# Kernel tuning notes

Measured on AMD Instinct MI355X. Metric: run time of the kernel, lower is better.

Reference implementation:

```python
import jax, jax.numpy as jnp
import numpy as np

B, S, D, H = 2, 2048, 1024, 16
HD = D // H  # head size 64

def setup_inputs() -> dict:
    key = jax.random.key(0)
    ks = jax.random.split(key, 7)
    sc = 1.0 / np.sqrt(D)
    return {
        "batch_data": jax.random.normal(ks[0], (B, S, D), dtype=jnp.float32),
        "Wq": jax.random.normal(ks[1], (D, D), dtype=jnp.float32) * sc,
        "bq": jnp.zeros((D,), dtype=jnp.float32),
        "Wk": jax.random.normal(ks[2], (D, D), dtype=jnp.float32) * sc,
        "bk": jnp.zeros((D,), dtype=jnp.float32),
        "Wv": jax.random.normal(ks[3], (D, D), dtype=jnp.float32) * sc,
        "bv": jnp.zeros((D,), dtype=jnp.float32),
    }

def _split_heads(x):
    # [B,S,D] -> [B,H,S,HD]
    b, s, _ = x.shape
    return x.reshape(b, s, H, HD).transpose(0, 2, 1, 3)

def reference(batch_data, Wq, bq, Wk, bk, Wv, bv):
    q = _split_heads(batch_data @ Wq + bq)
    k = _split_heads(batch_data @ Wk + bk)
    v = _split_heads(batch_data @ Wv + bv)
    scores = jnp.einsum('bhqd,bhkd->bhqk', q, k) / jnp.sqrt(jnp.float32(HD))
    probs = jax.nn.softmax(scores, axis=-1)
    ctx = jnp.einsum('bhqk,bhkd->bhqd', probs, v)  # [B,H,S,HD]
    ctx = ctx.transpose(0, 2, 1, 3).reshape(batch_data.shape[0], batch_data.shape[1], D)
    return jnp.mean(ctx, axis=1)  # mean pool over sequence -> [B,D]
```

## Files before the change

kernel.cpp:

```cpp
#include <hip/hip_runtime.h>
#include <hip/hip_bf16.h>
#include <stdint.h>

#define B_  2
#define S_  2048
#define D_  1024
#define H_  16
#define HD_ 64

typedef __attribute__((ext_vector_type(8)))  __bf16 bf16x8;
typedef __attribute__((ext_vector_type(4)))  __bf16 bf16x4;
typedef __attribute__((ext_vector_type(2)))  __bf16 bf16x2;
typedef __attribute__((ext_vector_type(4)))  float  f32x4;
typedef __attribute__((ext_vector_type(16))) float  f32x16;
typedef __attribute__((ext_vector_type(4)))  uint32_t u32x4;

#define QSCALE 0.18033688011112042f

__device__ __forceinline__ void gload16(const void* g, void* l) {
  __builtin_amdgcn_global_load_lds(
      (__attribute__((address_space(1))) void*)(uintptr_t)g,
      (__attribute__((address_space(3))) void*)(uintptr_t)l,
      16, 0, 0);
}

__device__ __forceinline__ uint32_t pkbf(float a, float b) {
  bf16x2 p; p[0] = (__bf16)a; p[1] = (__bf16)b;
  return __builtin_bit_cast(uint32_t, p);
}

__global__ __launch_bounds__(256) void zero_out_k(float* out) {
  int i = blockIdx.x * 256 + threadIdx.x;
  if (i < B_ * D_) out[i] = 0.0f;
}

__global__ __launch_bounds__(256) void convert_x(const float* __restrict__ x,
                                                 __bf16* __restrict__ xb) {
  int i = blockIdx.x * 256 + threadIdx.x;
  float4 v = ((const float4*)x)[i];
  bf16x4 o;
  o[0] = (__bf16)v.x; o[1] = (__bf16)v.y; o[2] = (__bf16)v.z; o[3] = (__bf16)v.w;
  ((bf16x4*)xb)[i] = o;
}

__global__ __launch_bounds__(256) void transpose_w(const float* __restrict__ wq,
                                                   const float* __restrict__ wk,
                                                   const float* __restrict__ wv,
                                                   __bf16* __restrict__ wt) {
  __shared__ float tile[32][33];
  const float* w = (blockIdx.z == 0) ? wq : (blockIdx.z == 1 ? wk : wv);
  __bf16* o = wt + (size_t)blockIdx.z * D_ * D_;
  int k0 = blockIdx.y * 32, n0 = blockIdx.x * 32;
  int tx = threadIdx.x, ty = threadIdx.y;
  for (int i = 0; i < 4; ++i)
    tile[ty + 8 * i][tx] = w[(size_t)(k0 + ty + 8 * i) * D_ + n0 + tx];
  __syncthreads();
  for (int i = 0; i < 4; ++i)
    o[(size_t)(n0 + ty + 8 * i) * D_ + k0 + tx] = (__bf16)tile[tx][ty + 8 * i];
}

__global__ __launch_bounds__(256, 3) void gemm_qkv(
    const __bf16* __restrict__ xb, const __bf16* __restrict__ wt,
    const float* __restrict__ bq, const float* __restrict__ bk,
    const float* __restrict__ bv, __bf16* __restrict__ qh,
    __bf16* __restrict__ kh, __bf16* __restrict__ vt) {
  constexpr int K = 1024;
  __shared__ __attribute__((aligned(16))) __bf16 lA[128 * 64];
  __shared__ __attribute__((aligned(16))) __bf16 lB[128 * 64];

  const int z = blockIdx.z;
  const __bf16* w = wt + (size_t)z * K * D_;
  const float* bias = (z == 0) ? bq : (z == 1 ? bk : bv);
  const int t = threadIdx.x;
  const int lane = t & 63;
  const int wid = t >> 6;
  const int quad = lane >> 4;
  const int col = lane & 15;
  const int m0 = blockIdx.x * 128;
  const int n0 = blockIdx.y * 128;
  const int wr = (wid >> 1) * 64;
  const int wc = (wid & 1) * 64;

  const int gc = (t & 7) ^ ((t >> 3) & 7);

  f32x4 acc[4][4] = {};

  if (z < 2) {
    for (int kt = 0; kt < K / 64; ++kt) {
      __syncthreads();
      for (int r = 0; r < 4; ++r) {
        int row = r * 32 + (t >> 3);
        gload16(xb + (size_t)(m0 + row) * K + kt * 64 + gc * 8,
                (char*)lA + r * 4096 + t * 16);
        gload16(w + (size_t)(n0 + row) * K + kt * 64 + gc * 8,
                (char*)lB + r * 4096 + t * 16);
      }
      __syncthreads();
      for (int ks = 0; ks < 2; ++ks) {
        bf16x8 fw[4], fx[4];
        for (int i = 0; i < 4; ++i) {
          int n = wr + i * 16 + col;
          int ch = (ks * 4 + quad) ^ (n & 7);
          fw[i] = *(const bf16x8*)((const char*)lB + n * 128 + ch * 16);
        }
        for (int j = 0; j < 4; ++j) {
          int m = wc + j * 16 + col;
          int ch = (ks * 4 + quad) ^ (m & 7);
          fx[j] = *(const bf16x8*)((const char*)lA + m * 128 + ch * 16);
        }
        for (int i = 0; i < 4; ++i)
          for (int j = 0; j < 4; ++j)
            acc[i][j] = __builtin_amdgcn_mfma_f32_16x16x32_bf16(
                fw[i], fx[j], acc[i][j], 0, 0, 0);
      }
    }
    const float scale = (z == 0) ? QSCALE : 1.0f;
    __bf16* dst = (z == 0) ? qh : kh;
    for (int i = 0; i < 4; ++i) {
      int gnb = n0 + wr + i * 16 + quad * 4;
      float4 bi = *(const float4*)(bias + gnb);
      int h = gnb >> 6, hd = gnb & 63;
      for (int j = 0; j < 4; ++j) {
        int gm = m0 + wc + j * 16 + col;
        int b = gm >> 11, s = gm & 2047;
        bf16x4 pk;
        pk[0] = (__bf16)((acc[i][j][0] + bi.x) * scale);
        pk[1] = (__bf16)((acc[i][j][1] + bi.y) * scale);
        pk[2] = (__bf16)((acc[i][j][2] + bi.z) * scale);
        pk[3] = (__bf16)((acc[i][j][3] + bi.w) * scale);
        *(bf16x4*)(dst + ((size_t)(b * H_ + h) * S_ + s) * HD_ + hd) = pk;
      }
    }
  } else {
    for (int kt = 0; kt < K / 64; ++kt) {
      __syncthreads();
      for (int r = 0; r < 4; ++r) {
        int row = r * 32 + (t >> 3);
        gload16(xb + (size_t)(m0 + row) * K + kt * 64 + gc * 8,
                (char*)lA + r * 4096 + t * 16);
        gload16(w + (size_t)(n0 + row) * K + kt * 64 + gc * 8,
                (char*)lB + r * 4096 + t * 16);
      }
      __syncthreads();
      for (int ks = 0; ks < 2; ++ks) {
        bf16x8 fx[4], fw[4];
        for (int i = 0; i < 4; ++i) {
          int m = wr + i * 16 + col;
          int ch = (ks * 4 + quad) ^ (m & 7);
          fx[i] = *(const bf16x8*)((const char*)lA + m * 128 + ch * 16);
        }
        for (int j = 0; j < 4; ++j) {
          int n = wc + j * 16 + col;
          int ch = (ks * 4 + quad) ^ (n & 7);
          fw[j] = *(const bf16x8*)((const char*)lB + n * 128 + ch * 16);
        }
        for (int i = 0; i < 4; ++i)
          for (int j = 0; j < 4; ++j)
            acc[i][j] = __builtin_amdgcn_mfma_f32_16x16x32_bf16(
                fx[i], fw[j], acc[i][j], 0, 0, 0);
      }
    }
    for (int i = 0; i < 4; ++i) {
      int gmb = m0 + wr + i * 16 + quad * 4;
      int b = gmb >> 11, s = gmb & 2047;
      for (int j = 0; j < 4; ++j) {
        int gn = n0 + wc + j * 16 + col;
        int h = gn >> 6, hd = gn & 63;
        float bi = bias[gn];
        bf16x4 pk;
        pk[0] = (__bf16)(acc[i][j][0] + bi);
        pk[1] = (__bf16)(acc[i][j][1] + bi);
        pk[2] = (__bf16)(acc[i][j][2] + bi);
        pk[3] = (__bf16)(acc[i][j][3] + bi);
        *(bf16x4*)(vt + ((size_t)(b * H_ + h) * HD_ + hd) * S_ + s) = pk;
      }
    }
  }
}

__global__ __launch_bounds__(256, 2) void attn(const __bf16* __restrict__ qh,
                                               const __bf16* __restrict__ kh,
                                               const __bf16* __restrict__ vt,
                                               float* __restrict__ out) {
  __shared__ __attribute__((aligned(16))) __bf16 lK[128 * 64];
  __shared__ __attribute__((aligned(16))) __bf16 lV[64 * 128];

  const int t = threadIdx.x;
  const int lane = t & 63;
  const int wid = t >> 6;
  const int half = lane >> 5;
  const int q31 = lane & 31;
  const int bh = blockIdx.x;
  const int q0w = blockIdx.y * 128 + wid * 32;

  const __bf16* qbase = qh + (size_t)bh * S_ * HD_;
  const __bf16* kbase = kh + (size_t)bh * S_ * HD_;
  const __bf16* vbase = vt + (size_t)bh * HD_ * S_;

  bf16x8 aq[4];
  for (int ks = 0; ks < 4; ++ks)
    aq[ks] = *(const bf16x8*)(qbase + (size_t)(q0w + q31) * HD_ + ks * 16 + half * 8);

  f32x16 o[2] = {};
  float lsum = 0.f;

  const int kslot = t & 7,  kgc = kslot ^ ((t >> 3) & 7);
  const int vslot = t & 15, vgc = vslot ^ ((t >> 4) & 15);

  for (int kt = 0; kt < S_ / 128; ++kt) {
    __syncthreads();
    for (int r = 0; r < 4; ++r) {
      int row = r * 32 + (t >> 3);
      gload16(kbase + (size_t)(kt * 128 + row) * HD_ + kgc * 8,
              (char*)lK + r * 4096 + t * 16);
      int rowv = r * 16 + (t >> 4);
      gload16(vbase + (size_t)rowv * S_ + kt * 128 + vgc * 8,
              (char*)lV + r * 4096 + t * 16);
    }
    __syncthreads();

    for (int st = 0; st < 4; ++st) {
      f32x16 sc = {};
      for (int ks = 0; ks < 4; ++ks) {
        int row = st * 32 + q31;
        int ch = (ks * 2 + half) ^ (row & 7);
        bf16x8 fk = *(const bf16x8*)((const char*)lK + row * 128 + ch * 16);
        sc = __builtin_amdgcn_mfma_f32_32x32x16_bf16(fk, aq[ks], sc, 0, 0, 0);
      }

      float e[16];
      for (int r = 0; r < 16; ++r) e[r] = exp2f(sc[r]);
      for (int r = 0; r < 16; ++r) lsum += e[r];
      uint32_t pk[8], x[8];
      for (int p = 0; p < 8; ++p) pk[p] = pkbf(e[2 * p], e[2 * p + 1]);
      for (int p = 0; p < 8; ++p) x[p] = __shfl_xor((int)pk[p], 32);

      bool h1 = (half != 0);
      u32x4 f0 = {h1 ? x[2] : pk[0], h1 ? x[3] : pk[1],
                  h1 ? pk[2] : x[0], h1 ? pk[3] : x[1]};
      u32x4 f1 = {h1 ? x[6] : pk[4], h1 ? x[7] : pk[5],
                  h1 ? pk[6] : x[4], h1 ? pk[7] : x[5]};
      bf16x8 Fa = __builtin_bit_cast(bf16x8, f0);
      bf16x8 Fb = __builtin_bit_cast(bf16x8, f1);

      for (int hdt = 0; hdt < 2; ++hdt) {
        int rowv = hdt * 32 + q31;
        int ch0 = (st * 4 + half) ^ (rowv & 15);
        int ch1 = (st * 4 + 2 + half) ^ (rowv & 15);
        bf16x8 fv0 = *(const bf16x8*)((const char*)lV + rowv * 256 + ch0 * 16);
        bf16x8 fv1 = *(const bf16x8*)((const char*)lV + rowv * 256 + ch1 * 16);
        o[hdt] = __builtin_amdgcn_mfma_f32_32x32x16_bf16(fv0, Fa, o[hdt], 0, 0, 0);
        o[hdt] = __builtin_amdgcn_mfma_f32_32x32x16_bf16(fv1, Fb, o[hdt], 0, 0, 0);
      }
    }
  }

  float ltot = lsum + __shfl_xor(lsum, 32);
  float linv = 1.0f / ltot;
  const int b = bh >> 4, h = bh & 15;
  for (int hdt = 0; hdt < 2; ++hdt)
    for (int r = 0; r < 16; ++r) {
      float v = o[hdt][r] * linv;
      v += __shfl_xor(v, 1);
      v += __shfl_xor(v, 2);
      v += __shfl_xor(v, 4);
      v += __shfl_xor(v, 8);
      v += __shfl_xor(v, 16);
      if (q31 == 0) {
        int hd = hdt * 32 + (r & 3) + 8 * (r >> 2) + 4 * half;
        atomicAdd(out + (size_t)b * D_ + h * HD_ + hd, v * (1.0f / S_));
      }
    }
}

extern "C" void kernel_launch(void* const* d_in, const int* in_sizes, int n_in,
                              void* d_out, int out_size, void* d_ws, size_t ws_size,
                              hipStream_t stream) {
  const float* x  = (const float*)d_in[0];
  const float* Wq = (const float*)d_in[1];
  const float* bq = (const float*)d_in[2];
  const float* Wk = (const float*)d_in[3];
  const float* bk = (const float*)d_in[4];
  const float* Wv = (const float*)d_in[5];
  const float* bv = (const float*)d_in[6];
  float* out = (float*)d_out;

  char* ws = (char*)d_ws;
  __bf16* qh = (__bf16*)(ws);
  __bf16* kh = (__bf16*)(ws + ((size_t)8  << 20));
  __bf16* vt = (__bf16*)(ws + ((size_t)16 << 20));
  __bf16* xb = (__bf16*)(ws + ((size_t)24 << 20));
  __bf16* wt = (__bf16*)(ws + ((size_t)32 << 20));

  zero_out_k<<<dim3((B_ * D_ + 255) / 256), dim3(256), 0, stream>>>(out);
  convert_x<<<dim3((B_ * S_ * D_) / 1024), dim3(256), 0, stream>>>(x, xb);
  transpose_w<<<dim3(32, 32, 3), dim3(32, 8), 0, stream>>>(Wq, Wk, Wv, wt);
  gemm_qkv<<<dim3(32, 8, 3), dim3(256), 0, stream>>>(xb, wt, bq, bk, bv, qh, kh, vt);
  attn<<<dim3(B_ * H_, S_ / 128), dim3(256), 0, stream>>>(qh, kh, vt, out);
}
```

Baseline: 191.5 us.

## Double-buffer K/V tiles in LDS and split MFMA accumulator chains

```diff
diff --git a/kernel.cpp b/kernel.cpp
--- a/kernel.cpp
+++ b/kernel.cpp
@@ -182,16 +182,15 @@
                                                const __bf16* __restrict__ kh,
                                                const __bf16* __restrict__ vt,
                                                float* __restrict__ out) {
-  __shared__ __attribute__((aligned(16))) __bf16 lK[128 * 64];
-  __shared__ __attribute__((aligned(16))) __bf16 lV[64 * 128];
+  __shared__ __attribute__((aligned(16))) __bf16 lK[2][128 * 64];
+  __shared__ __attribute__((aligned(16))) __bf16 lV[2][64 * 128];
 
   const int t = threadIdx.x;
   const int lane = t & 63;
-  const int wid = t >> 6;
   const int half = lane >> 5;
   const int q31 = lane & 31;
   const int bh = blockIdx.x;
-  const int q0w = blockIdx.y * 128 + wid * 32;
+  const int q0w = blockIdx.y * 128 + (t >> 6) * 32;
 
   const __bf16* qbase = qh + (size_t)bh * S_ * HD_;
   const __bf16* kbase = kh + (size_t)bh * S_ * HD_;
@@ -201,40 +200,54 @@
   for (int ks = 0; ks < 4; ++ks)
     aq[ks] = *(const bf16x8*)(qbase + (size_t)(q0w + q31) * HD_ + ks * 16 + half * 8);
 
-  f32x16 o[2] = {};
-  float lsum = 0.f;
-
-  const int kslot = t & 7,  kgc = kslot ^ ((t >> 3) & 7);
-  const int vslot = t & 15, vgc = vslot ^ ((t >> 4) & 15);
-
-  for (int kt = 0; kt < S_ / 128; ++kt) {
-    __syncthreads();
+  const int kgc = (t & 7) ^ ((t >> 3) & 7);
+  const int vgc = (t & 15) ^ ((t >> 4) & 15);
+
+  auto stage = [&](int kt, int buf) {
     for (int r = 0; r < 4; ++r) {
       int row = r * 32 + (t >> 3);
       gload16(kbase + (size_t)(kt * 128 + row) * HD_ + kgc * 8,
-              (char*)lK + r * 4096 + t * 16);
+              (char*)&lK[buf][0] + r * 4096 + t * 16);
       int rowv = r * 16 + (t >> 4);
       gload16(vbase + (size_t)rowv * S_ + kt * 128 + vgc * 8,
-              (char*)lV + r * 4096 + t * 16);
-    }
+              (char*)&lV[buf][0] + r * 4096 + t * 16);
+    }
+  };
+
+  f32x16 o[2][2] = {};
+  float lsum = 0.f;
+
+  stage(0, 0);
+
+  for (int kt = 0; kt < S_ / 128; ++kt) {
+    const int cur = kt & 1;
     __syncthreads();
-
+    if (kt + 1 < S_ / 128) stage(kt + 1, cur ^ 1);
+
+    f32x16 sc[4] = {};
+#pragma unroll
     for (int st = 0; st < 4; ++st) {
-      f32x16 sc = {};
+      int row = st * 32 + q31;
+#pragma unroll
       for (int ks = 0; ks < 4; ++ks) {
-        int row = st * 32 + q31;
         int ch = (ks * 2 + half) ^ (row & 7);
-        bf16x8 fk = *(const bf16x8*)((const char*)lK + row * 128 + ch * 16);
-        sc = __builtin_amdgcn_mfma_f32_32x32x16_bf16(fk, aq[ks], sc, 0, 0, 0);
-      }
-
+        bf16x8 fk = *(const bf16x8*)((const char*)&lK[cur][0] + row * 128 + ch * 16);
+        sc[st] = __builtin_amdgcn_mfma_f32_32x32x16_bf16(fk, aq[ks], sc[st], 0, 0, 0);
+      }
+    }
+
+#pragma unroll
+    for (int st = 0; st < 4; ++st) {
       float e[16];
-      for (int r = 0; r < 16; ++r) e[r] = exp2f(sc[r]);
+#pragma unroll
+      for (int r = 0; r < 16; ++r) e[r] = exp2f(sc[st][r]);
+#pragma unroll
       for (int r = 0; r < 16; ++r) lsum += e[r];
       uint32_t pk[8], x[8];
+#pragma unroll
       for (int p = 0; p < 8; ++p) pk[p] = pkbf(e[2 * p], e[2 * p + 1]);
+#pragma unroll
       for (int p = 0; p < 8; ++p) x[p] = __shfl_xor((int)pk[p], 32);
-
       bool h1 = (half != 0);
       u32x4 f0 = {h1 ? x[2] : pk[0], h1 ? x[3] : pk[1],
                   h1 ? pk[2] : x[0], h1 ? pk[3] : x[1]};
@@ -242,15 +255,17 @@
                   h1 ? pk[6] : x[4], h1 ? pk[7] : x[5]};
       bf16x8 Fa = __builtin_bit_cast(bf16x8, f0);
       bf16x8 Fb = __builtin_bit_cast(bf16x8, f1);
-
+#pragma unroll
       for (int hdt = 0; hdt < 2; ++hdt) {
         int rowv = hdt * 32 + q31;
         int ch0 = (st * 4 + half) ^ (rowv & 15);
         int ch1 = (st * 4 + 2 + half) ^ (rowv & 15);
-        bf16x8 fv0 = *(const bf16x8*)((const char*)lV + rowv * 256 + ch0 * 16);
-        bf16x8 fv1 = *(const bf16x8*)((const char*)lV + rowv * 256 + ch1 * 16);
-        o[hdt] = __builtin_amdgcn_mfma_f32_32x32x16_bf16(fv0, Fa, o[hdt], 0, 0, 0);
-        o[hdt] = __builtin_amdgcn_mfma_f32_32x32x16_bf16(fv1, Fb, o[hdt], 0, 0, 0);
+        bf16x8 fv0 = *(const bf16x8*)((const char*)&lV[cur][0] + rowv * 256 + ch0 * 16);
+        bf16x8 fv1 = *(const bf16x8*)((const char*)&lV[cur][0] + rowv * 256 + ch1 * 16);
+        o[hdt][st & 1] = __builtin_amdgcn_mfma_f32_32x32x16_bf16(
+            fv0, Fa, o[hdt][st & 1], 0, 0, 0);
+        o[hdt][st & 1] = __builtin_amdgcn_mfma_f32_32x32x16_bf16(
+            fv1, Fb, o[hdt][st & 1], 0, 0, 0);
       }
     }
   }
@@ -258,9 +273,11 @@
   float ltot = lsum + __shfl_xor(lsum, 32);
   float linv = 1.0f / ltot;
   const int b = bh >> 4, h = bh & 15;
+#pragma unroll
   for (int hdt = 0; hdt < 2; ++hdt)
+#pragma unroll
     for (int r = 0; r < 16; ++r) {
-      float v = o[hdt][r] * linv;
+      float v = (o[hdt][0][r] + o[hdt][1][r]) * linv;
       v += __shfl_xor(v, 1);
       v += __shfl_xor(v, 2);
       v += __shfl_xor(v, 4);
```

Result: no change. 189.7 us (-1.0%).

## Double-buffer QKV GEMM loads and split attention across two key chunks

Applied to the files above, without the earlier changes.

```diff
diff --git a/kernel.cpp b/kernel.cpp
--- a/kernel.cpp
+++ b/kernel.cpp
@@ -65,8 +65,9 @@
     const float* __restrict__ bv, __bf16* __restrict__ qh,
     __bf16* __restrict__ kh, __bf16* __restrict__ vt) {
   constexpr int K = 1024;
-  __shared__ __attribute__((aligned(16))) __bf16 lA[128 * 64];
-  __shared__ __attribute__((aligned(16))) __bf16 lB[128 * 64];
+  constexpr int NIT = K / 32;
+  __shared__ __attribute__((aligned(16))) __bf16 lA[2][128 * 32];
+  __shared__ __attribute__((aligned(16))) __bf16 lB[2][128 * 32];
 
   const int z = blockIdx.z;
   const __bf16* w = wt + (size_t)z * K * D_;
@@ -81,38 +82,44 @@
   const int wr = (wid >> 1) * 64;
   const int wc = (wid & 1) * 64;
 
-  const int gc = (t & 7) ^ ((t >> 3) & 7);
+  const int sr0 = t >> 2;
+  const int gc = (t & 3) ^ ((t >> 2) & 3);
+
+  auto stage = [&](int kt, int buf) {
+    gload16(xb + (size_t)(m0 + sr0) * K + kt * 32 + gc * 8,
+            (char*)&lA[buf][0] + t * 16);
+    gload16(xb + (size_t)(m0 + 64 + sr0) * K + kt * 32 + gc * 8,
+            (char*)&lA[buf][0] + 4096 + t * 16);
+    gload16(w + (size_t)(n0 + sr0) * K + kt * 32 + gc * 8,
+            (char*)&lB[buf][0] + t * 16);
+    gload16(w + (size_t)(n0 + 64 + sr0) * K + kt * 32 + gc * 8,
+            (char*)&lB[buf][0] + 4096 + t * 16);
+  };
 
   f32x4 acc[4][4] = {};
 
+  stage(0, 0);
+
   if (z < 2) {
-    for (int kt = 0; kt < K / 64; ++kt) {
+    for (int kt = 0; kt < NIT; ++kt) {
+      const int cur = kt & 1;
       __syncthreads();
-      for (int r = 0; r < 4; ++r) {
-        int row = r * 32 + (t >> 3);
-        gload16(xb + (size_t)(m0 + row) * K + kt * 64 + gc * 8,
-                (char*)lA + r * 4096 + t * 16);
-        gload16(w + (size_t)(n0 + row) * K + kt * 64 + gc * 8,
-                (char*)lB + r * 4096 + t * 16);
-      }
-      __syncthreads();
-      for (int ks = 0; ks < 2; ++ks) {
-        bf16x8 fw[4], fx[4];
-        for (int i = 0; i < 4; ++i) {
-          int n = wr + i * 16 + col;
-          int ch = (ks * 4 + quad) ^ (n & 7);
-          fw[i] = *(const bf16x8*)((const char*)lB + n * 128 + ch * 16);
-        }
-        for (int j = 0; j < 4; ++j) {
-          int m = wc + j * 16 + col;
-          int ch = (ks * 4 + quad) ^ (m & 7);
-          fx[j] = *(const bf16x8*)((const char*)lA + m * 128 + ch * 16);
-        }
-        for (int i = 0; i < 4; ++i)
-          for (int j = 0; j < 4; ++j)
-            acc[i][j] = __builtin_amdgcn_mfma_f32_16x16x32_bf16(
-                fw[i], fx[j], acc[i][j], 0, 0, 0);
-      }
+      if (kt + 1 < NIT) stage(kt + 1, cur ^ 1);
+      bf16x8 fw[4], fx[4];
+      for (int i = 0; i < 4; ++i) {
+        int n = wr + i * 16 + col;
+        int sl = quad ^ (n & 3);
+        fw[i] = *(const bf16x8*)((const char*)&lB[cur][0] + n * 64 + sl * 16);
+      }
+      for (int j = 0; j < 4; ++j) {
+        int m = wc + j * 16 + col;
+        int sl = quad ^ (m & 3);
+        fx[j] = *(const bf16x8*)((const char*)&lA[cur][0] + m * 64 + sl * 16);
+      }
+      for (int i = 0; i < 4; ++i)
+        for (int j = 0; j < 4; ++j)
+          acc[i][j] = __builtin_amdgcn_mfma_f32_16x16x32_bf16(
+              fw[i], fx[j], acc[i][j], 0, 0, 0);
     }
     const float scale = (z == 0) ? QSCALE : 1.0f;
     __bf16* dst = (z == 0) ? qh : kh;
@@ -132,33 +139,25 @@
       }
     }
   } else {
-    for (int kt = 0; kt < K / 64; ++kt) {
+    for (int kt = 0; kt < NIT; ++kt) {
+      const int cur = kt & 1;
       __syncthreads();
-      for (int r = 0; r < 4; ++r) {
-        int row = r * 32 + (t >> 3);
-        gload16(xb + (size_t)(m0 + row) * K + kt * 64 + gc * 8,
-                (char*)lA + r * 4096 + t * 16);
-        gload16(w + (size_t)(n0 + row) * K + kt * 64 + gc * 8,
-                (char*)lB + r * 4096 + t * 16);
-      }
-      __syncthreads();
-      for (int ks = 0; ks < 2; ++ks) {
-        bf16x8 fx[4], fw[4];
-        for (int i = 0; i < 4; ++i) {
-          int m = wr + i * 16 + col;
-          int ch = (ks * 4 + quad) ^ (m & 7);
-          fx[i] = *(const bf16x8*)((const char*)lA + m * 128 + ch * 16);
-        }
-        for (int j = 0; j < 4; ++j) {
-          int n = wc + j * 16 + col;
-          int ch = (ks * 4 + quad) ^ (n & 7);
-          fw[j] = *(const bf16x8*)((const char*)lB + n * 128 + ch * 16);
-        }
-        for (int i = 0; i < 4; ++i)
-          for (int j = 0; j < 4; ++j)
-            acc[i][j] = __builtin_amdgcn_mfma_f32_16x16x32_bf16(
-                fx[i], fw[j], acc[i][j], 0, 0, 0);
-      }
+      if (kt + 1 < NIT) stage(kt + 1, cur ^ 1);
+      bf16x8 fx[4], fw[4];
+      for (int i = 0; i < 4; ++i) {
+        int m = wr + i * 16 + col;
+        int sl = quad ^ (m & 3);
+        fx[i] = *(const bf16x8*)((const char*)&lA[cur][0] + m * 64 + sl * 16);
+      }
+      for (int j = 0; j < 4; ++j) {
+        int n = wc + j * 16 + col;
+        int sl = quad ^ (n & 3);
+        fw[j] = *(const bf16x8*)((const char*)&lB[cur][0] + n * 64 + sl * 16);
+      }
+      for (int i = 0; i < 4; ++i)
+        for (int j = 0; j < 4; ++j)
+          acc[i][j] = __builtin_amdgcn_mfma_f32_16x16x32_bf16(
+              fx[i], fw[j], acc[i][j], 0, 0, 0);
     }
     for (int i = 0; i < 4; ++i) {
       int gmb = m0 + wr + i * 16 + quad * 4;
@@ -178,20 +177,20 @@
   }
 }
 
-__global__ __launch_bounds__(256, 2) void attn(const __bf16* __restrict__ qh,
-                                               const __bf16* __restrict__ kh,
-                                               const __bf16* __restrict__ vt,
-                                               float* __restrict__ out) {
+__global__ __launch_bounds__(256, 4) void attn1(
+    const __bf16* __restrict__ qh, const __bf16* __restrict__ kh,
+    const __bf16* __restrict__ vt, __bf16* __restrict__ po,
+    float* __restrict__ pl) {
   __shared__ __attribute__((aligned(16))) __bf16 lK[128 * 64];
   __shared__ __attribute__((aligned(16))) __bf16 lV[64 * 128];
 
   const int t = threadIdx.x;
   const int lane = t & 63;
-  const int wid = t >> 6;
   const int half = lane >> 5;
   const int q31 = lane & 31;
   const int bh = blockIdx.x;
-  const int q0w = blockIdx.y * 128 + wid * 32;
+  const int kc = blockIdx.z;
+  const int q0w = blockIdx.y * 128 + (t >> 6) * 32;
 
   const __bf16* qbase = qh + (size_t)bh * S_ * HD_;
   const __bf16* kbase = kh + (size_t)bh * S_ * HD_;
@@ -204,10 +203,10 @@
   f32x16 o[2] = {};
   float lsum = 0.f;
 
-  const int kslot = t & 7,  kgc = kslot ^ ((t >> 3) & 7);
-  const int vslot = t & 15, vgc = vslot ^ ((t >> 4) & 15);
-
-  for (int kt = 0; kt < S_ / 128; ++kt) {
+  const int kgc = (t & 7) ^ ((t >> 3) & 7);
+  const int vgc = (t & 15) ^ ((t >> 4) & 15);
+
+  for (int kt = kc * 8; kt < kc * 8 + 8; ++kt) {
     __syncthreads();
     for (int r = 0; r < 4; ++r) {
       int row = r * 32 + (t >> 3);
@@ -256,21 +255,46 @@
   }
 
   float ltot = lsum + __shfl_xor(lsum, 32);
-  float linv = 1.0f / ltot;
-  const int b = bh >> 4, h = bh & 15;
+  const size_t slab = (size_t)(kc * 32 + bh) * S_;
+  const int qrow = q0w + q31;
+  if (half == 0) pl[slab + qrow] = ltot;
   for (int hdt = 0; hdt < 2; ++hdt)
-    for (int r = 0; r < 16; ++r) {
-      float v = o[hdt][r] * linv;
-      v += __shfl_xor(v, 1);
-      v += __shfl_xor(v, 2);
-      v += __shfl_xor(v, 4);
-      v += __shfl_xor(v, 8);
-      v += __shfl_xor(v, 16);
-      if (q31 == 0) {
-        int hd = hdt * 32 + (r & 3) + 8 * (r >> 2) + 4 * half;
-        atomicAdd(out + (size_t)b * D_ + h * HD_ + hd, v * (1.0f / S_));
-      }
-    }
+    for (int rq = 0; rq < 4; ++rq) {
+      bf16x4 pk;
+      pk[0] = (__bf16)o[hdt][rq * 4 + 0];
+      pk[1] = (__bf16)o[hdt][rq * 4 + 1];
+      pk[2] = (__bf16)o[hdt][rq * 4 + 2];
+      pk[3] = (__bf16)o[hdt][rq * 4 + 3];
+      *(bf16x4*)(po + (slab + qrow) * HD_ + hdt * 32 + rq * 8 + half * 4) = pk;
+    }
+}
+
+__global__ __launch_bounds__(256) void attn2(const __bf16* __restrict__ po,
+                                             const float* __restrict__ pl,
+                                             float* __restrict__ out) {
+  __shared__ float red[256];
+  const int t = threadIdx.x;
+  const int hd = t & 63;
+  const int rgrp = t >> 6;
+  const int bh = blockIdx.y;
+  const int r0 = blockIdx.x * 256 + rgrp * 64;
+  const size_t s0 = (size_t)bh * S_;
+  const size_t s1 = (size_t)(32 + bh) * S_;
+  float acc = 0.f;
+  for (int i = 0; i < 64; ++i) {
+    int row = r0 + i;
+    float l = pl[s0 + row] + pl[s1 + row];
+    float v = (float)po[(s0 + row) * HD_ + hd] +
+              (float)po[(s1 + row) * HD_ + hd];
+    acc += v / l;
+  }
+  red[t] = acc;
+  __syncthreads();
+  if (t < 64) {
+    float s = red[t] + red[t + 64] + red[t + 128] + red[t + 192];
+    atomicAdd(out + (size_t)(bh >> 4) * D_ + (bh & 15) * HD_ + hd,
+              s * (1.0f / S_));
+  }
 }
 
 extern "C" void kernel_launch(void* const* d_in, const int* in_sizes, int n_in,
@@ -291,10 +315,13 @@
   __bf16* vt = (__bf16*)(ws + ((size_t)16 << 20));
   __bf16* xb = (__bf16*)(ws + ((size_t)24 << 20));
   __bf16* wt = (__bf16*)(ws + ((size_t)32 << 20));
+  __bf16* po = (__bf16*)(ws + ((size_t)24 << 20));
+  float*  pl = (float*) (ws + ((size_t)40 << 20));
 
   zero_out_k<<<dim3((B_ * D_ + 255) / 256), dim3(256), 0, stream>>>(out);
   convert_x<<<dim3((B_ * S_ * D_) / 1024), dim3(256), 0, stream>>>(x, xb);
   transpose_w<<<dim3(32, 32, 3), dim3(32, 8), 0, stream>>>(Wq, Wk, Wv, wt);
   gemm_qkv<<<dim3(32, 8, 3), dim3(256), 0, stream>>>(xb, wt, bq, bk, bv, qh, kh, vt);
-  attn<<<dim3(B_ * H_, S_ / 128), dim3(256), 0, stream>>>(qh, kh, vt, out);
-}
+  attn1<<<dim3(B_ * H_, S_ / 128, 2), dim3(256), 0, stream>>>(qh, kh, vt, po, pl);
+  attn2<<<dim3(8, B_ * H_), dim3(256), 0, stream>>>(po, pl, out);
+}
```

Result: faster. 181.4 us (-5.3%).
